# Performance work log

Measured on AMD Instinct MI355X. Metric: run time of the kernel, lower is better.

Reference implementation:

```python
import jax, jax.numpy as jnp
import numpy as np


def _conv1x1(W, x):
    # W: (out_c, in_c) from a 1x1 Conv2d (bias=False); x: (b, in_c, h, w)
    return jnp.einsum('oc,bchw->bohw', W, x)


def setup_inputs() -> dict:
    key = jax.random.key(0)
    ks = jax.random.split(key, 7)
    b, c, h, w = 4, 256, 64, 64
    inter = c // 2
    out_c = 256
    s = 0.02
    return {
        'A': jax.random.normal(ks[0], (b, c, h, w), dtype=jnp.float32),
        'B': jax.random.normal(ks[1], (b, c, h, w), dtype=jnp.float32),
        'W_phi': jax.random.normal(ks[2], (inter, c), dtype=jnp.float32) * s,
        'W_theta': jax.random.normal(ks[3], (inter, c), dtype=jnp.float32) * s,
        'W_g': jax.random.normal(ks[4], (inter, 2 * c), dtype=jnp.float32) * s,
        'W_AB': jax.random.normal(ks[5], (out_c, 2 * c), dtype=jnp.float32) * s,
        'W_mask': jax.random.normal(ks[6], (out_c, inter), dtype=jnp.float32) * s,
    }


def reference(A, B, W_phi, W_theta, W_g, W_AB, W_mask):
    b, c, h, w = A.shape
    inter = c // 2
    AB = jnp.concatenate([A, B], axis=1)  # (b, 2c, h, w)
    # NOTE: original torch code views (b, c/2, h*w) as (b, c, h*w/2) -> seq len N = h*w/2
    x_phi = _conv1x1(W_phi, A).reshape(b, c, -1)                       # (b, c, N)
    x_theta = _conv1x1(W_theta, B).reshape(b, c, -1).transpose(0, 2, 1)  # (b, N, c)
    x_g = _conv1x1(W_g, AB).reshape(b, c, -1).transpose(0, 2, 1)       # (b, N, c)
    scores = jnp.einsum('bnc,bcm->bnm', x_theta, x_phi)                # (b, N, N)
    attn = jax.nn.softmax(scores, axis=1)  # softmax over dim=1 as in torch code
    y = jnp.einsum('bnm,bmc->bnc', attn, x_g)                          # (b, N, c)
    y = y.transpose(0, 2, 1).reshape(b, inter, h, w)
    out = _conv1x1(W_mask, y) + _conv1x1(W_AB, AB)
    return out
```

## Files before the change

### kernel.cpp

```cpp
#include <hip/hip_runtime.h>
#include <hip/hip_bf16.h>

#define B_    4
#define C_    256
#define HW    4096
#define N_    2048
#define BSTR  524288

typedef unsigned short u16;
using f32x4 = __attribute__((ext_vector_type(4))) float;
using u32x4 = __attribute__((ext_vector_type(4))) unsigned int;

__device__ __forceinline__ float bf2f(u16 u) {
    return __uint_as_float(((unsigned)u) << 16);
}
__device__ __forceinline__ u16 f2bf(float f) {
    unsigned x = __float_as_uint(f);
    x += 0x7fff + ((x >> 16) & 1);
    return (u16)(x >> 16);
}

__device__ __forceinline__ void mfma_bf16(f32x4& acc, u32x4 a, u32x4 b) {
    asm volatile("v_mfma_f32_16x16x32_bf16 %0, %1, %2, %0"
                 : "+v"(acc) : "v"(a), "v"(b));
}
__device__ __forceinline__ void mfma_bf16_vsrc(f32x4& acc, u32x4 a, u32x4 b) {
    asm volatile("s_nop 1\n\tv_mfma_f32_16x16x32_bf16 %0, %1, %2, %0"
                 : "+v"(acc) : "v"(a), "v"(b));
}
__device__ __forceinline__ void mfma_fence(f32x4& x) {
    asm volatile("s_nop 7\n\ts_nop 7" : "+v"(x));
}

__global__ __launch_bounds__(256) void prep_w(
    const float* __restrict__ Wphi, const float* __restrict__ Wtheta,
    const float* __restrict__ Wg, const float* __restrict__ Wab,
    u16* __restrict__ Wt)
{
    const int row = blockIdx.x;
    const int t   = threadIdx.x;
    #pragma unroll
    for (int i = 0; i < 2; ++i) {
        const int col = i * 256 + t;
        float v;
        if (row < 128)      v = (col < 256)  ? Wphi[row * 256 + col] : 0.f;
        else if (row < 256) v = (col >= 256) ? Wtheta[(row - 128) * 256 + (col - 256)] : 0.f;
        else if (row < 384) v = Wg[(row - 256) * 512 + col];
        else                v = Wab[(row - 384) * 512 + col];
        Wt[row * 512 + col] = f2bf(v);
    }
}

__global__ __launch_bounds__(256) void prep_abt(
    const float* __restrict__ A, const float* __restrict__ Bx,
    u16* __restrict__ ABt)
{
    __shared__ u16 L[64][528];
    const int t = threadIdx.x, pb = blockIdx.x, b = blockIdx.y;
    const int p0 = pb * 64;
    const int pl = t & 63, cg = t >> 6;
    const float* Ab = A  + (size_t)b * C_ * HW;
    const float* Bb = Bx + (size_t)b * C_ * HW;

    for (int i = 0; i < 64; ++i) {
        const int c = cg + i * 4;
        L[pl][c]       = f2bf(Ab[c * HW + p0 + pl]);
        L[pl][256 + c] = f2bf(Bb[c * HW + p0 + pl]);
    }
    __syncthreads();
    u16* dst = ABt + ((size_t)b * 4096 + p0) * 512;
    #pragma unroll
    for (int i = 0; i < 16; ++i) {
        const int idx = i * 256 + t;
        const int row = idx >> 6, ch = idx & 63;
        *(uint4*)&dst[row * 512 + ch * 8] = *(const uint4*)&L[row][ch * 8];
    }
}

__global__ __launch_bounds__(256) void conv_gemm(
    const u16* __restrict__ Wt, const u16* __restrict__ ABt,
    u16* __restrict__ phit, u16* __restrict__ thetat,
    u16* __restrict__ g, float* __restrict__ out)
{
    __shared__ __align__(16) u16 shW[64 * 128];
    __shared__ __align__(16) u16 shAB[64 * 128];
    const int t = threadIdx.x, pb = blockIdx.x, nb = blockIdx.y, b = blockIdx.z;
    const int lane = t & 63, w = t >> 6, lo = lane & 15, hi = lane >> 4;
    const u16* Wb = Wt + nb * 64 * 512;
    const u16* Ab = ABt + ((size_t)b * 4096 + pb * 64) * 512;

    f32x4 acc[4];
    #pragma unroll
    for (int ot = 0; ot < 4; ++ot) acc[ot] = (f32x4){0.f, 0.f, 0.f, 0.f};

    for (int ks = 0; ks < 4; ++ks) {
        __syncthreads();
        #pragma unroll
        for (int i = 0; i < 4; ++i) {
            const int q = i * 256 + t;
            const int row = q >> 4, c16 = (q & 15) * 8;
            const int sw = (row & 7) << 3;
            *(uint4*)&shW[row * 128 + (c16 ^ sw)]  = *(const uint4*)&Wb[row * 512 + ks * 128 + c16];
            *(uint4*)&shAB[row * 128 + (c16 ^ sw)] = *(const uint4*)&Ab[row * 512 + ks * 128 + c16];
        }
        __syncthreads();
        u32x4 bfr[4];
        {
            const int row = w * 16 + lo, sw = (row & 7) << 3;
            #pragma unroll
            for (int kf = 0; kf < 4; ++kf)
                bfr[kf] = *(const u32x4*)&shAB[row * 128 + ((kf * 32 + hi * 8) ^ sw)];
        }
        #pragma unroll
        for (int ot = 0; ot < 4; ++ot) {
            const int row = ot * 16 + lo, sw = (row & 7) << 3;
            #pragma unroll
            for (int kf = 0; kf < 4; ++kf) {
                const u32x4 a = *(const u32x4*)&shW[row * 128 + ((kf * 32 + hi * 8) ^ sw)];
                mfma_bf16(acc[ot], a, bfr[kf]);
            }
        }
    }

    const int p_global = pb * 64 + w * 16 + lo;
    const int m = p_global & 2047, h = p_global >> 11;
    #pragma unroll
    for (int ot = 0; ot < 4; ++ot) {
        mfma_fence(acc[ot]);
        const int ob = nb * 64 + ot * 16 + hi * 4;
        if (nb < 2) {
            ushort4 v;
            v.x = f2bf(acc[ot][0]); v.y = f2bf(acc[ot][1]);
            v.z = f2bf(acc[ot][2]); v.w = f2bf(acc[ot][3]);
            *(ushort4*)&phit[(size_t)b * BSTR + m * 256 + h * 128 + ob] = v;
        } else if (nb < 4) {
            ushort4 v;
            v.x = f2bf(acc[ot][0]); v.y = f2bf(acc[ot][1]);
            v.z = f2bf(acc[ot][2]); v.w = f2bf(acc[ot][3]);
            *(ushort4*)&thetat[(size_t)b * BSTR + m * 256 + h * 128 + (ob - 128)] = v;
        } else if (nb < 6) {
            #pragma unroll
            for (int q = 0; q < 4; ++q)
                g[(size_t)b * BSTR + (ob - 256 + q) * HW + p_global] = f2bf(acc[ot][q]);
        } else {
            #pragma unroll
            for (int q = 0; q < 4; ++q)
                out[(size_t)b * C_ * HW + (size_t)(ob - 384 + q) * HW + p_global] = acc[ot][q];
        }
    }
}

__global__ __launch_bounds__(256) void passA_mfma(
    const u16* __restrict__ phit, const u16* __restrict__ thetat,
    float* __restrict__ rs)
{
    __shared__ __align__(16) u16 shP[64 * 256];
    __shared__ __align__(16) u16 shT[64 * 256];
    const int t = threadIdx.x, b = blockIdx.z, nq = blockIdx.y, mb = blockIdx.x;
    const u16* Pb = phit   + b * BSTR + mb * 64 * 256;
    const u16* Tb = thetat + b * BSTR + nq * 512 * 256;

    #pragma unroll
    for (int i = 0; i < 8; ++i) {
        const int q = i * 256 + t;
        const int row = q >> 5, c16 = (q & 31) * 8;
        const uint4 v = *(const uint4*)&Pb[row * 256 + c16];
        *(uint4*)&shP[row * 256 + (c16 ^ ((row & 7) << 3))] = v;
    }
    __syncthreads();

    const int lane = t & 63, w = t >> 6, lo = lane & 15, hi = lane >> 4;
    u32x4 afr[8];
    {
        const int row = w * 16 + lo;
        #pragma unroll
        for (int kb = 0; kb < 8; ++kb)
            afr[kb] = *(const u32x4*)&shP[row * 256 + ((kb * 32 + hi * 8) ^ ((row & 7) << 3))];
    }

    float rsacc[4] = {0.f, 0.f, 0.f, 0.f};
    for (int nt = 0; nt < 8; ++nt) {
        __syncthreads();
        #pragma unroll
        for (int i = 0; i < 8; ++i) {
            const int q = i * 256 + t;
            const int row = q >> 5, c16 = (q & 31) * 8;
            const uint4 v = *(const uint4*)&Tb[(nt * 64 + row) * 256 + c16];
            *(uint4*)&shT[row * 256 + (c16 ^ ((row & 7) << 3))] = v;
        }
        __syncthreads();
        #pragma unroll
        for (int ns = 0; ns < 4; ++ns) {
            f32x4 acc = {0.f, 0.f, 0.f, 0.f};
            const int row = ns * 16 + lo;
            #pragma unroll
            for (int kb = 0; kb < 8; ++kb) {
                const u32x4 bfr = *(const u32x4*)&shT[row * 256 + ((kb * 32 + hi * 8) ^ ((row & 7) << 3))];
                mfma_bf16(acc, afr[kb], bfr);
            }
            mfma_fence(acc);
            rsacc[0] += __expf(acc.x); rsacc[1] += __expf(acc.y);
            rsacc[2] += __expf(acc.z); rsacc[3] += __expf(acc.w);
        }
    }
    #pragma unroll
    for (int q = 0; q < 4; ++q) {
        float v = rsacc[q];
        v += __shfl_xor(v, 1); v += __shfl_xor(v, 2);
        v += __shfl_xor(v, 4); v += __shfl_xor(v, 8);
        rsacc[q] = v;
    }
    if (lo == 0) {
        const int m = mb * 64 + w * 16 + hi * 4;
        float* dst = rs + (nq * 4 + b) * N_ + m;
        dst[0] = rsacc[0]; dst[1] = rsacc[1]; dst[2] = rsacc[2]; dst[3] = rsacc[3];
    }
}

__global__ __launch_bounds__(256) void g_scale(
    const float* __restrict__ rs, u16* __restrict__ g)
{
    const int t  = threadIdx.x;
    const int mt = blockIdx.x;
    const int cg = blockIdx.y;
    const int b  = blockIdx.z;
    const int m  = mt * 256 + t;
    const float* rp = rs + b * N_ + m;
    const float inv = 1.0f / (rp[0] + rp[8192] + rp[16384] + rp[24576]);
    u16* gb = g + (size_t)b * BSTR + cg * 8 * N_ + m;
    #pragma unroll
    for (int j = 0; j < 8; ++j)
        gb[j * N_] = f2bf(bf2f(gb[j * N_]) * inv);
}

__global__ __launch_bounds__(256) void passB_mfma(
    const u16* __restrict__ phit, const u16* __restrict__ thetat,
    const u16* __restrict__ g, u16* __restrict__ ytp)
{
    __shared__ __align__(16) u16 shBuf[64 * 256];
    u16* shT  = shBuf;
    u16* shPm = shBuf;
    u16* shG  = shBuf + 32 * 256;

    const int t = threadIdx.x, b = blockIdx.z, mh = blockIdx.y, nb = blockIdx.x;
    const u16* Tb = thetat + b * BSTR + nb * 64 * 256;
    const u16* Pb = phit   + b * BSTR + mh * 1024 * 256;
    const u16* Gb = g      + b * BSTR;
    const int lane = t & 63, w = t >> 6, lo = lane & 15, hi = lane >> 4;

    #pragma unroll
    for (int i = 0; i < 8; ++i) {
        const int q = i * 256 + t;
        const int row = q >> 5, c16 = (q & 31) * 8;
        const uint4 v = *(const uint4*)&Tb[row * 256 + c16];
        *(uint4*)&shT[row * 256 + (c16 ^ ((row & 7) << 3))] = v;
    }
    __syncthreads();
    u32x4 bfr[8];
    {
        const int row = w * 16 + lo;
        #pragma unroll
        for (int kb = 0; kb < 8; ++kb)
            bfr[kb] = *(const u32x4*)&shT[row * 256 + ((kb * 32 + hi * 8) ^ ((row & 7) << 3))];
    }
    __syncthreads();

    f32x4 accY[16];
    #pragma unroll
    for (int ct = 0; ct < 16; ++ct) accY[ct] = (f32x4){0.f, 0.f, 0.f, 0.f};

    uint4 vp[4], vg[4];
    #pragma unroll
    for (int i = 0; i < 4; ++i) {
        const int q = i * 256 + t;
        vp[i] = *(const uint4*)&Pb[(q >> 5) * 256 + (q & 31) * 8];
    }
    #pragma unroll
    for (int qd = 0; qd < 4; ++qd)
        vg[qd] = *(const uint4*)&Gb[(size_t)t * N_ + mh * 1024 + qd * 8];

    for (int mt = 0; mt < 32; ++mt) {
        __syncthreads();
        #pragma unroll
        for (int i = 0; i < 4; ++i) {
            const int q = i * 256 + t;
            const int row = q >> 5, c16 = (q & 31) * 8;
            *(uint4*)&shPm[row * 256 + (c16 ^ ((row & 7) << 3))] = vp[i];
        }
        {
            const int sw = (t & 7) << 2, base = t * 32;
            #pragma unroll
            for (int qd = 0; qd < 4; ++qd) {
                const int m0 = qd * 8;
                *(uint2*)&shG[base + ((m0    ) ^ sw)] = make_uint2(vg[qd].x, vg[qd].y);
                *(uint2*)&shG[base + ((m0 + 4) ^ sw)] = make_uint2(vg[qd].z, vg[qd].w);
            }
        }
        const int mtn = (mt < 31) ? mt + 1 : 31;
        uint4 vp2[4], vg2[4];
        #pragma unroll
        for (int i = 0; i < 4; ++i) {
            const int q = i * 256 + t;
            vp2[i] = *(const uint4*)&Pb[(mtn * 32 + (q >> 5)) * 256 + (q & 31) * 8];
        }
        #pragma unroll
        for (int qd = 0; qd < 4; ++qd)
            vg2[qd] = *(const uint4*)&Gb[(size_t)t * N_ + mh * 1024 + mtn * 32 + qd * 8];
        __syncthreads();

        f32x4 s0 = {0.f, 0.f, 0.f, 0.f}, s1 = {0.f, 0.f, 0.f, 0.f};
        {
            const int row = lo;
            #pragma unroll
            for (int kb = 0; kb < 8; ++kb) {
                const u32x4 a = *(const u32x4*)&shPm[row * 256 + ((kb * 32 + hi * 8) ^ ((row & 7) << 3))];
                mfma_bf16(s0, a, bfr[kb]);
            }
        }
        {
            const int row = 16 + lo;
            #pragma unroll
            for (int kb = 0; kb < 8; ++kb) {
                const u32x4 a = *(const u32x4*)&shPm[row * 256 + ((kb * 32 + hi * 8) ^ ((row & 7) << 3))];
                mfma_bf16(s1, a, bfr[kb]);
            }
        }
        mfma_fence(s0); mfma_fence(s1);

        float p0[4], p1[4];
        #pragma unroll
        for (int q = 0; q < 4; ++q) {
            p0[q] = __expf(s0[q]);
            p1[q] = __expf(s1[q]);
        }
        u32x4 pf;
        pf[0] = (unsigned)f2bf(p0[0]) | ((unsigned)f2bf(p0[1]) << 16);
        pf[1] = (unsigned)f2bf(p0[2]) | ((unsigned)f2bf(p0[3]) << 16);
        pf[2] = (unsigned)f2bf(p1[0]) | ((unsigned)f2bf(p1[1]) << 16);
        pf[3] = (unsigned)f2bf(p1[2]) | ((unsigned)f2bf(p1[3]) << 16);

        #pragma unroll
        for (int ct = 0; ct < 16; ++ct) {
            const int row = ct * 16 + lo;
            const int sw = (row & 7) << 2, m4 = hi * 4;
            const uint2 a0 = *(const uint2*)&shG[row * 32 + ((m4     ) ^ sw)];
            const uint2 a1 = *(const uint2*)&shG[row * 32 + ((16 + m4) ^ sw)];
            u32x4 gf; gf[0] = a0.x; gf[1] = a0.y; gf[2] = a1.x; gf[3] = a1.y;
            mfma_bf16_vsrc(accY[ct], gf, pf);
        }

        #pragma unroll
        for (int i = 0; i < 4; ++i) vp[i] = vp2[i];
        #pragma unroll
        for (int qd = 0; qd < 4; ++qd) vg[qd] = vg2[qd];
    }

    u16* Yb = ytp + ((size_t)mh * B_ + b) * BSTR;
    const int col = nb * 64 + w * 16 + lo;
    #pragma unroll
    for (int ct = 0; ct < 16; ++ct) {
        mfma_fence(accY[ct]);
        const int crow = ct * 16 + hi * 4;
        #pragma unroll
        for (int q = 0; q < 4; ++q)
            Yb[(crow + q) * N_ + col] = f2bf(accY[ct][q]);
    }
}

__global__ __launch_bounds__(256) void mask_add_kernel(
    const u16* __restrict__ ytp, const float* __restrict__ Wm,
    float* __restrict__ out)
{
    const int p  = blockIdx.x * 256 + threadIdx.x;
    const int og = blockIdx.y;
    const int b  = blockIdx.z;
    const u16* Y0 = ytp + (size_t)b * BSTR;
    const u16* Y1 = ytp + ((size_t)B_ + b) * BSTR;

    float acc[8] = {};
    for (int k = 0; k < 128; ++k) {
        const float y = bf2f(Y0[k * HW + p]) + bf2f(Y1[k * HW + p]);
        #pragma unroll
        for (int j = 0; j < 8; ++j)
            acc[j] = fmaf(Wm[(og * 8 + j) * 128 + k], y, acc[j]);
    }
    float* ob = out + (size_t)b * C_ * HW;
    #pragma unroll
    for (int j = 0; j < 8; ++j)
        ob[(og * 8 + j) * HW + p] += acc[j];
}

extern "C" void kernel_launch(void* const* d_in, const int* in_sizes, int n_in,
                              void* d_out, int out_size, void* d_ws, size_t ws_size,
                              hipStream_t stream)
{
    const float* A      = (const float*)d_in[0];
    const float* Bx     = (const float*)d_in[1];
    const float* Wphi   = (const float*)d_in[2];
    const float* Wtheta = (const float*)d_in[3];
    const float* Wg     = (const float*)d_in[4];
    const float* Wab    = (const float*)d_in[5];
    const float* Wmask  = (const float*)d_in[6];
    float* out = (float*)d_out;

    u16*   ABt    = (u16*)d_ws;
    u16*   ytp    = ABt;
    float* rs     = (float*)(ABt + 4194304);
    u16*   Wt     = ABt + 8388608;
    u16*   phit   = Wt + 327680;
    u16*   thetat = phit + 2097152;
    u16*   g      = thetat + 2097152;

    prep_w<<<dim3(640), 256, 0, stream>>>(Wphi, Wtheta, Wg, Wab, Wt);

    prep_abt<<<dim3(64, 4), 256, 0, stream>>>(A, Bx, ABt);

    conv_gemm<<<dim3(64, 10, 4), 256, 0, stream>>>(
        Wt, ABt, phit, thetat, g, out);

    passA_mfma<<<dim3(32, 4, 4), 256, 0, stream>>>(phit, thetat, rs);

    g_scale<<<dim3(8, 32, 4), 256, 0, stream>>>(rs, g);

    passB_mfma<<<dim3(32, 2, 4), 256, 0, stream>>>(phit, thetat, g, ytp);

    mask_add_kernel<<<dim3(16, 32, 4), 256, 0, stream>>>(ytp, Wmask, out);
}
```

Measured before the change: 284.6 us.

## Split passB over four m-quarters with double-buffered LDS and padded G layout

passB now splits the m dimension into four parts instead of two, doubling the grid to 512 blocks for better CU occupancy. Its partial outputs go to four ytp slices, which mask_add sums, and rs moves so it does not overlap the larger ytp. The shared memory is double-buffered so one barrier per iteration is removed, the G tile uses a padded stride of 36 in place of the XOR swizzle, and s_setprio is raised around the MFMA sections. This costs extra partial-output traffic and more reads in mask_add, and the larger LDS footprint may limit how many blocks fit per CU.

```diff
diff --git a/kernel.cpp b/kernel.cpp
--- a/kernel.cpp
+++ b/kernel.cpp
@@ -237,17 +237,14 @@
     const u16* __restrict__ phit, const u16* __restrict__ thetat,
     const u16* __restrict__ g, u16* __restrict__ ytp)
 {
-    __shared__ __align__(16) u16 shBuf[64 * 256];
-    u16* shT  = shBuf;
-    u16* shPm = shBuf;
-    u16* shG  = shBuf + 32 * 256;
-
-    const int t = threadIdx.x, b = blockIdx.z, mh = blockIdx.y, nb = blockIdx.x;
+    __shared__ __align__(16) u16 shBuf[2][17408];
+    const int t = threadIdx.x, b = blockIdx.z, mq = blockIdx.y, nb = blockIdx.x;
     const u16* Tb = thetat + b * BSTR + nb * 64 * 256;
-    const u16* Pb = phit   + b * BSTR + mh * 1024 * 256;
-    const u16* Gb = g      + b * BSTR;
+    const u16* Pb = phit   + b * BSTR + mq * 512 * 256;
+    const u16* Gb = g      + b * BSTR + mq * 512;
     const int lane = t & 63, w = t >> 6, lo = lane & 15, hi = lane >> 4;
 
+    u16* shT = &shBuf[0][0];
     #pragma unroll
     for (int i = 0; i < 8; ++i) {
         const int q = i * 256 + t;
@@ -277,10 +274,12 @@
     }
     #pragma unroll
     for (int qd = 0; qd < 4; ++qd)
-        vg[qd] = *(const uint4*)&Gb[(size_t)t * N_ + mh * 1024 + qd * 8];
-
-    for (int mt = 0; mt < 32; ++mt) {
-        __syncthreads();
+        vg[qd] = *(const uint4*)&Gb[(size_t)t * N_ + qd * 8];
+
+    for (int mt = 0; mt < 16; ++mt) {
+        u16* shPm = &shBuf[mt & 1][0];
+        u16* shG  = &shBuf[mt & 1][8192];
+
         #pragma unroll
         for (int i = 0; i < 4; ++i) {
             const int q = i * 256 + t;
@@ -288,26 +287,29 @@
             *(uint4*)&shPm[row * 256 + (c16 ^ ((row & 7) << 3))] = vp[i];
         }
         {
-            const int sw = (t & 7) << 2, base = t * 32;
-            #pragma unroll
-            for (int qd = 0; qd < 4; ++qd) {
-                const int m0 = qd * 8;
-                *(uint2*)&shG[base + ((m0    ) ^ sw)] = make_uint2(vg[qd].x, vg[qd].y);
-                *(uint2*)&shG[base + ((m0 + 4) ^ sw)] = make_uint2(vg[qd].z, vg[qd].w);
-            }
-        }
-        const int mtn = (mt < 31) ? mt + 1 : 31;
-        uint4 vp2[4], vg2[4];
+            u16* gr = &shG[t * 36];
+            *(uint2*)&gr[0]  = make_uint2(vg[0].x, vg[0].y);
+            *(uint2*)&gr[4]  = make_uint2(vg[0].z, vg[0].w);
+            *(uint2*)&gr[8]  = make_uint2(vg[1].x, vg[1].y);
+            *(uint2*)&gr[12] = make_uint2(vg[1].z, vg[1].w);
+            *(uint2*)&gr[16] = make_uint2(vg[2].x, vg[2].y);
+            *(uint2*)&gr[20] = make_uint2(vg[2].z, vg[2].w);
+            *(uint2*)&gr[24] = make_uint2(vg[3].x, vg[3].y);
+            *(uint2*)&gr[28] = make_uint2(vg[3].z, vg[3].w);
+        }
+        const int mtn = (mt < 15) ? mt + 1 : 15;
         #pragma unroll
         for (int i = 0; i < 4; ++i) {
             const int q = i * 256 + t;
-            vp2[i] = *(const uint4*)&Pb[(mtn * 32 + (q >> 5)) * 256 + (q & 31) * 8];
+            vp[i] = *(const uint4*)&Pb[(mtn * 32 + (q >> 5)) * 256 + (q & 31) * 8];
         }
         #pragma unroll
         for (int qd = 0; qd < 4; ++qd)
-            vg2[qd] = *(const uint4*)&Gb[(size_t)t * N_ + mh * 1024 + mtn * 32 + qd * 8];
+            vg[qd] = *(const uint4*)&Gb[(size_t)t * N_ + mtn * 32 + qd * 8];
+
         __syncthreads();
 
+        __builtin_amdgcn_s_setprio(1);
         f32x4 s0 = {0.f, 0.f, 0.f, 0.f}, s1 = {0.f, 0.f, 0.f, 0.f};
         {
             const int row = lo;
@@ -325,6 +327,7 @@
                 mfma_bf16(s1, a, bfr[kb]);
             }
         }
+        __builtin_amdgcn_s_setprio(0);
         mfma_fence(s0); mfma_fence(s1);
 
         float p0[4], p1[4];
@@ -339,23 +342,20 @@
         pf[2] = (unsigned)f2bf(p1[0]) | ((unsigned)f2bf(p1[1]) << 16);
         pf[3] = (unsigned)f2bf(p1[2]) | ((unsigned)f2bf(p1[3]) << 16);
 
+        __builtin_amdgcn_s_setprio(1);
         #pragma unroll
         for (int ct = 0; ct < 16; ++ct) {
             const int row = ct * 16 + lo;
-            const int sw = (row & 7) << 2, m4 = hi * 4;
-            const uint2 a0 = *(const uint2*)&shG[row * 32 + ((m4     ) ^ sw)];
-            const uint2 a1 = *(const uint2*)&shG[row * 32 + ((16 + m4) ^ sw)];
+            const uint2 a0 = *(const uint2*)&shG[row * 36 + hi * 4];
+            const uint2 a1 = *(const uint2*)&shG[row * 36 + 16 + hi * 4];
             u32x4 gf; gf[0] = a0.x; gf[1] = a0.y; gf[2] = a1.x; gf[3] = a1.y;
-            mfma_bf16_vsrc(accY[ct], gf, pf);
-        }
-
-        #pragma unroll
-        for (int i = 0; i < 4; ++i) vp[i] = vp2[i];
-        #pragma unroll
-        for (int qd = 0; qd < 4; ++qd) vg[qd] = vg2[qd];
-    }
-
-    u16* Yb = ytp + ((size_t)mh * B_ + b) * BSTR;
+            if (ct == 0) mfma_bf16_vsrc(accY[ct], gf, pf);
+            else         mfma_bf16(accY[ct], gf, pf);
+        }
+        __builtin_amdgcn_s_setprio(0);
+    }
+
+    u16* Yb = ytp + ((size_t)mq * B_ + b) * BSTR;
     const int col = nb * 64 + w * 16 + lo;
     #pragma unroll
     for (int ct = 0; ct < 16; ++ct) {
@@ -374,12 +374,15 @@
     const int p  = blockIdx.x * 256 + threadIdx.x;
     const int og = blockIdx.y;
     const int b  = blockIdx.z;
-    const u16* Y0 = ytp + (size_t)b * BSTR;
-    const u16* Y1 = ytp + ((size_t)B_ + b) * BSTR;
+    const u16* Y0 = ytp + (size_t)(0 * B_ + b) * BSTR;
+    const u16* Y1 = ytp + (size_t)(1 * B_ + b) * BSTR;
+    const u16* Y2 = ytp + (size_t)(2 * B_ + b) * BSTR;
+    const u16* Y3 = ytp + (size_t)(3 * B_ + b) * BSTR;
 
     float acc[8] = {};
     for (int k = 0; k < 128; ++k) {
-        const float y = bf2f(Y0[k * HW + p]) + bf2f(Y1[k * HW + p]);
+        const float y = bf2f(Y0[k * HW + p]) + bf2f(Y1[k * HW + p])
+                      + bf2f(Y2[k * HW + p]) + bf2f(Y3[k * HW + p]);
         #pragma unroll
         for (int j = 0; j < 8; ++j)
             acc[j] = fmaf(Wm[(og * 8 + j) * 128 + k], y, acc[j]);
@@ -405,11 +408,11 @@
 
     u16*   ABt    = (u16*)d_ws;
     u16*   ytp    = ABt;
-    float* rs     = (float*)(ABt + 4194304);
     u16*   Wt     = ABt + 8388608;
     u16*   phit   = Wt + 327680;
     u16*   thetat = phit + 2097152;
     u16*   g      = thetat + 2097152;
+    float* rs     = (float*)(g + 2097152);
 
     prep_w<<<dim3(640), 256, 0, stream>>>(Wphi, Wtheta, Wg, Wab, Wt);
 
@@ -422,7 +425,7 @@
 
     g_scale<<<dim3(8, 32, 4), 256, 0, stream>>>(rs, g);
 
-    passB_mfma<<<dim3(32, 2, 4), 256, 0, stream>>>(phit, thetat, g, ytp);
+    passB_mfma<<<dim3(32, 4, 4), 256, 0, stream>>>(phit, thetat, g, ytp);
 
     mask_add_kernel<<<dim3(16, 32, 4), 256, 0, stream>>>(ytp, Wmask, out);
 }
```

Result: faster. 256.6 us (-9.8%).
